# Kernel tuning notes

Hardware: AMD Instinct MI355X
Metric: run time of the kernel (lower is better)

## Reference

```python
import jax, jax.numpy as jnp
import numpy as np

# ---- config (matches init_kwargs) ----
B, N_ENC, COND_REPEAT = 4, 4, 200
BLOCKS, LAYERS_PER = 2, 8
R, S, CC, CLASSES = 128, 128, 64, 256
Q_ZERO = 128
DILATIONS = [2 ** i for i in range(LAYERS_PER)] * BLOCKS  # [1..128, 1..128]
L = len(DILATIONS)


def setup_inputs() -> dict:
    key = jax.random.key(0)
    ks = jax.random.split(key, 12)
    g = lambda k, shape, fan: (jax.random.normal(k, shape, jnp.float32) / np.float32(np.sqrt(fan)))
    return {
        "encodings": jax.random.normal(ks[0], (B, CC, N_ENC), jnp.float32),
        "W_first": g(ks[1], (R, 1, 2), 2.0),            # causal conv 1->R, k=2
        "b_first": jnp.zeros((R,), jnp.float32),
        "Wc": g(ks[2], (L, 2 * R, R, 2), 2.0 * R),       # dilated causal convs R->2R, k=2
        "bc": jnp.zeros((L, 2 * R), jnp.float32),
        "Wcond": g(ks[3], (L, 2 * R, CC), CC),           # per-layer 1x1 cond (no bias)
        "Wres": g(ks[4], (L, R, R), R),                  # per-layer 1x1 residual
        "bres": jnp.zeros((L, R), jnp.float32),
        "Wskip_l": g(ks[5], (L, S, R), R),               # per-layer 1x1 skip
        "bskip_l": jnp.zeros((L, S), jnp.float32),
        "Wskip0": g(ks[6], (S, R), R),                   # top skip_conv
        "bskip0": jnp.zeros((S,), jnp.float32),
        "Wcond_top": g(ks[7], (S, CC), CC),              # top 1x1 cond (no bias)
        "Wfc": g(ks[8], (S, S), S),
        "bfc": jnp.zeros((S,), jnp.float32),
        "Wlogits": g(ks[9], (CLASSES, S), S),
        "blogits": jnp.zeros((CLASSES,), jnp.float32),
    }


def reference(encodings, W_first, b_first, Wc, bc, Wcond, Wres, bres,
              Wskip_l, bskip_l, Wskip0, bskip0, Wcond_top, Wfc, bfc,
              Wlogits, blogits):
    """Autoregressive WaveNet generation with per-layer dilated-conv queues.
    Returns per-step logits [B, CLASSES, T] (sampling uses argmax, method='max')."""
    T = N_ENC * COND_REPEAT
    # each encoding frame conditions cond_repeat consecutive samples
    c_seq = jnp.repeat(encodings, COND_REPEAT, axis=2).transpose(2, 0, 1)  # [T,B,CC]

    def step(carry, c_t):
        sample, fq, queues = carry  # sample:[B] int, fq:[B] (first-conv queue), queues: tuple of [B,R,d_l]
        x = sample.astype(jnp.float32) / 127.5 - 1.0  # mu-law index -> [-1, 1]
        # first causal conv (k=2): past value from queue, current value x
        res = fq[:, None] * W_first[:, 0, 0] + x[:, None] * W_first[:, 0, 1] + b_first  # [B,R]
        skip = res @ Wskip0.T + bskip0  # [B,S]
        new_queues = []
        for l in range(L):  # fixed structural loop over layers
            q = queues[l]  # [B,R,d_l]; q[:,:,0] is the input from d_l steps ago
            z = q[:, :, 0] @ Wc[l, :, :, 0].T + res @ Wc[l, :, :, 1].T + bc[l]  # [B,2R]
            z = z + c_t @ Wcond[l].T
            gate, out = jnp.split(z, 2, axis=1)
            h = jax.nn.sigmoid(gate) * jnp.tanh(out)
            new_queues.append(jnp.concatenate([q[:, :, 1:], res[:, :, None]], axis=2))
            skip = skip + h @ Wskip_l[l].T + bskip_l[l]
            res = res + h @ Wres[l].T + bres[l]  # residual connection
        s = jax.nn.relu(skip) @ Wfc.T + bfc + c_t @ Wcond_top.T
        logits = jax.nn.relu(s) @ Wlogits.T + blogits  # [B,CLASSES]
        new_sample = jnp.argmax(logits, axis=1).astype(jnp.int32)
        return (new_sample, x, tuple(new_queues)), logits

    carry0 = (jnp.full((B,), Q_ZERO, jnp.int32),
              jnp.zeros((B,), jnp.float32),
              tuple(jnp.zeros((B, R, d), jnp.float32) for d in DILATIONS))
    _, logits = jax.lax.scan(step, carry0, c_seq)
    return logits.transpose(1, 2, 0)  # [B, CLASSES, T]
```

## Files before the change

kernel.cpp:

```cpp
#include <hip/hip_runtime.h>


typedef unsigned long long u64;

#define TSTEPS 800
#define CREP 200

#define CTR_OFF 0
#define ABT_OFF 64
#define RESBOX_OFF 4096
#define BOXB 16384
#define SKIPBOX_OFF (RESBOX_OFF + 4 * BOXB)
#define RING_OFF (SKIPBOX_OFF + 4 * BOXB)
#define RINGB 261120
#define WS_END (RING_OFF + 4 * RINGB)

#define SPIN_LIMIT 1048576

static __device__ __forceinline__ void pub64(u64* p, float x, unsigned tag) {
  const u64 v = (u64)__float_as_uint(x) | ((u64)tag << 32);
  asm volatile("global_atomic_swap_x2 %0, %1, off" ::"v"(p), "v"(v) : "memory");
}
static __device__ __forceinline__ u64 poll64(u64* p) {
  u64 old;
  const u64 z = 0;
  asm volatile("global_atomic_add_x2 %0, %1, %2, off sc0\n\ts_waitcnt vmcnt(0)"
               : "=&v"(old) : "v"(p), "v"(z) : "memory");
  return old;
}
static __device__ __forceinline__ void poll4(u64* p, u64& a, u64& b, u64& c, u64& d) {
  const u64 z = 0;
  asm volatile(
      "global_atomic_add_x2 %0, %4, %5, off sc0\n\t"
      "global_atomic_add_x2 %1, %4, %5, off offset:1024 sc0\n\t"
      "global_atomic_add_x2 %2, %4, %5, off offset:2048 sc0\n\t"
      "global_atomic_add_x2 %3, %4, %5, off offset:3072 sc0\n\t"
      "s_waitcnt vmcnt(0)"
      : "=&v"(a), "=&v"(b), "=&v"(c), "=&v"(d)
      : "v"(p), "v"(z)
      : "memory");
}
static __device__ __forceinline__ unsigned ld32(const unsigned* p) {
  return __hip_atomic_load(p, __ATOMIC_RELAXED, __HIP_MEMORY_SCOPE_AGENT);
}
static __device__ __forceinline__ void st32(unsigned* p, unsigned v) {
  __hip_atomic_store(p, v, __ATOMIC_RELAXED, __HIP_MEMORY_SCOPE_AGENT);
}
static __device__ __forceinline__ float spinf(u64* p, unsigned tag, unsigned* abt) {
  int g = 0;
  for (;;) {
    const u64 v = poll64(p);
    if ((unsigned)(v >> 32) == tag) return __uint_as_float((unsigned)v);
    if (((++g) & 255) == 0) {
      if (g > SPIN_LIMIT || ld32(abt)) { st32(abt, 1u); return 0.f; }
    }
  }
}

__global__ void wn_init(unsigned char* ws) {
  uint4 z; z.x = 0; z.y = 0; z.z = 0; z.w = 0;
  uint4* p = (uint4*)ws;
  const int n = WS_END / 16;
  for (int i = blockIdx.x * blockDim.x + threadIdx.x; i < n; i += gridDim.x * blockDim.x)
    p[i] = z;
}

__global__ __launch_bounds__(512, 2) void wn_main(
    const float* __restrict__ enc, const float* __restrict__ Wfirst,
    const float* __restrict__ bfirst, const float* __restrict__ Wc,
    const float* __restrict__ bcv, const float* __restrict__ Wcond,
    const float* __restrict__ Wres, const float* __restrict__ bres,
    const float* __restrict__ Wskip, const float* __restrict__ bskipl,
    const float* __restrict__ Wskip0, const float* __restrict__ bskip0,
    const float* __restrict__ Wct, const float* __restrict__ Wfcw,
    const float* __restrict__ bfc, const float* __restrict__ Wlg,
    const float* __restrict__ blgg, float* __restrict__ dout,
    unsigned char* __restrict__ ws) {
  __shared__ __attribute__((aligned(16))) unsigned char smem[14336];
  float* zbS = (float*)smem;
  float* ct2 = (float*)smem;
  float* resS = (float*)(smem + 4096);
  float* zpartS = (float*)(smem + 4608);
  float* ppS = (float*)(smem + 6656);
  float* hS = (float*)(smem + 8704);
  float* rpartS = (float*)(smem + 9216);
  float* skpartS = (float*)(smem + 11264);
  float* pastS = (float*)(smem + 13312);
  float* amaxv = (float*)(smem + 13824);
  int* amaxi = (int*)(smem + 13840);
  int* argixS = (int*)(smem + 13856);
  int* roleS = (int*)(smem + 13872);

  const int tid = threadIdx.x;
  unsigned* abt = (unsigned*)(ws + ABT_OFF);

  if (tid == 0) {
    unsigned xcc;
    asm volatile("s_getreg_b32 %0, hwreg(HW_REG_XCC_ID)" : "=s"(xcc));
    int role = 999;
    if (xcc < 4)
      role = (int)__hip_atomic_fetch_add((unsigned*)(ws + CTR_OFF) + xcc, 1u,
                                         __ATOMIC_RELAXED, __HIP_MEMORY_SCOPE_AGENT);
    roleS[0] = role;
    roleS[1] = (int)xcc;
  }
  __syncthreads();
  const int role = roleS[0];
  const int b = roleS[1];
  if (role >= 17) return;

  const int jz = tid & 255, kh = tid >> 8;
  const int j3 = tid & 127, q3 = tid >> 7;

  if (role < 16) {
    const int l = role;
    const int dl = 1 << (l & 7);
    const int pfx = (l < 8) ? ((1 << l) - 1) : (254 + (1 << (l - 8)));

    float wc1h[64], wc0h[64], wresq[32];
    {
      const float4* wbase = (const float4*)(Wc + ((size_t)(l * 256 + jz) * 128 + kh * 64) * 2);
#pragma unroll
      for (int m = 0; m < 32; m++) {
        const float4 v = wbase[m];
        wc0h[2 * m] = v.x; wc1h[2 * m] = v.y;
        wc0h[2 * m + 1] = v.z; wc1h[2 * m + 1] = v.w;
      }
      const float4* rbase = (const float4*)(Wres + (size_t)(l * 128 + j3) * 128 + q3 * 32);
#pragma unroll
      for (int m = 0; m < 8; m++) {
        const float4 v = rbase[m];
        wresq[4 * m] = v.x; wresq[4 * m + 1] = v.y;
        wresq[4 * m + 2] = v.z; wresq[4 * m + 3] = v.w;
      }
    }
    const float bresv = bres[l * 128 + j3];

    if (tid < 256) {
      for (int e = 0; e < 4; e++) {
        float a = bcv[l * 256 + tid];
        for (int c = 0; c < 64; c++)
          a = fmaf(enc[(b * 64 + c) * 4 + e], Wcond[((size_t)l * 256 + tid) * 64 + c], a);
        zbS[e * 256 + tid] = a;
      }
    }
    ppS[tid] = 0.f;

    u64* inbox = (u64*)(ws + RESBOX_OFF + (size_t)b * BOXB) + l * 128;
    u64* outbox = (u64*)(ws + RESBOX_OFF + (size_t)b * BOXB) + ((l + 1) & 15) * 128;
    u64* skipbox = (u64*)(ws + SKIPBOX_OFF + (size_t)b * BOXB) + l * 128;
    float* ringf = (float*)(ws + RING_OFF + (size_t)b * RINGB) + pfx * 128;
    const float4* wskb = (const float4*)(Wskip + (size_t)(l * 128 + j3) * 128 + q3 * 32);
    __syncthreads();

    for (int t = 0; t < TSTEPS; t++) {
      const unsigned want = (unsigned)(t + 1);
      const int e = t / CREP;

      if (tid < 128) resS[tid] = spinf(inbox + tid, want, abt);
      __syncthreads();

      {
        const float* rp = resS + kh * 64;
        float zp = 0.f;
#pragma unroll
        for (int kk = 0; kk < 64; kk++) zp = fmaf(rp[kk], wc1h[kk], zp);
        zpartS[(kh << 8) | jz] = zp;
      }
      __syncthreads();
      if (tid < 128) {
        const float g0 = zpartS[tid] + zpartS[256 + tid] + ppS[tid] + ppS[256 + tid] +
                         zbS[e * 256 + tid];
        const float o0 = zpartS[128 + tid] + zpartS[384 + tid] + ppS[128 + tid] +
                         ppS[384 + tid] + zbS[e * 256 + 128 + tid];
        hS[tid] = (1.f / (1.f + expf(-g0))) * tanhf(o0);
      }
      __syncthreads();

      {
        const float* hp = hS + q3 * 32;
        float rp2 = 0.f;
#pragma unroll
        for (int kk = 0; kk < 32; kk++) rp2 = fmaf(hp[kk], wresq[kk], rp2);
        rpartS[(q3 << 7) | j3] = rp2;
      }
      __syncthreads();
      if (l < 15 && tid < 128)
        pub64(outbox + tid,
              resS[tid] + rpartS[tid] + rpartS[128 + tid] + rpartS[256 + tid] +
                  rpartS[384 + tid] + bresv,
              want);

      {
        const float* hp = hS + q3 * 32;
        float sp = 0.f;
#pragma unroll
        for (int m = 0; m < 8; m++) {
          const float4 wv = wskb[m];
          sp = fmaf(hp[4 * m], wv.x, sp);
          sp = fmaf(hp[4 * m + 1], wv.y, sp);
          sp = fmaf(hp[4 * m + 2], wv.z, sp);
          sp = fmaf(hp[4 * m + 3], wv.w, sp);
        }
        skpartS[(q3 << 7) | j3] = sp;
      }
      __syncthreads();
      if (tid < 128)
        pub64(skipbox + tid,
              skpartS[tid] + skpartS[128 + tid] + skpartS[256 + tid] + skpartS[384 + tid],
              want);

      if (tid < 128) {
        ringf[(t % dl) * 128 + tid] = resS[tid];
        pastS[tid] = (dl == 1) ? resS[tid] : ringf[((t + 1) % dl) * 128 + tid];
      }
      __syncthreads();
      {
        const float* pp2 = pastS + kh * 64;
        float ppn = 0.f;
#pragma unroll
        for (int kk = 0; kk < 64; kk++) ppn = fmaf(pp2[kk], wc0h[kk], ppn);
        ppS[(kh << 8) | jz] = ppn;
      }
    }
  } else {
    float wlgr[64], wfcr[32], wsk0[32];
    {
      const float4* lb = (const float4*)(Wlg + (size_t)jz * 128 + kh * 64);
#pragma unroll
      for (int m = 0; m < 16; m++) {
        const float4 v = lb[m];
        wlgr[4 * m] = v.x; wlgr[4 * m + 1] = v.y;
        wlgr[4 * m + 2] = v.z; wlgr[4 * m + 3] = v.w;
      }
      const float4* fb = (const float4*)(Wfcw + (size_t)j3 * 128 + q3 * 32);
      const float4* sb = (const float4*)(Wskip0 + (size_t)j3 * 128 + q3 * 32);
#pragma unroll
      for (int m = 0; m < 8; m++) {
        const float4 v = fb[m];
        const float4 u = sb[m];
        wfcr[4 * m] = v.x; wfcr[4 * m + 1] = v.y;
        wfcr[4 * m + 2] = v.z; wfcr[4 * m + 3] = v.w;
        wsk0[4 * m] = u.x; wsk0[4 * m + 1] = u.y;
        wsk0[4 * m + 2] = u.z; wsk0[4 * m + 3] = u.w;
      }
    }
    float wf0 = 0.f, wf1 = 0.f, bfv = 0.f, bs0 = 0.f, bsum = 0.f, bfcv = 0.f;
    if (tid < 128) {
      wf0 = Wfirst[2 * tid]; wf1 = Wfirst[2 * tid + 1]; bfv = bfirst[tid];
      bs0 = bskip0[tid];
      for (int l2 = 0; l2 < 16; l2++) bsum += bskipl[l2 * 128 + tid];
      bfcv = bfc[tid];
      for (int e = 0; e < 4; e++) {
        float a = 0.f;
        for (int c = 0; c < 64; c++)
          a = fmaf(enc[(b * 64 + c) * 4 + e], Wct[tid * 64 + c], a);
        ct2[e * 128 + tid] = a;
      }
    }
    const float blgv = (tid < 256) ? blgg[tid] : 0.f;
    float fq = 0.f, x = 128.f / 127.5f - 1.f;
    u64* res0box = (u64*)(ws + RESBOX_OFF + (size_t)b * BOXB);
    u64* skb = (u64*)(ws + SKIPBOX_OFF + (size_t)b * BOXB);
    float* res0S = resS;
    float* partS = zpartS;
    float* lgS = ppS;
    float* skS = hS;
    float* s1S = rpartS;
    __syncthreads();

    for (int t = 0; t < TSTEPS; t++) {
      const unsigned want = (unsigned)(t + 1);
      const int e = t / CREP;

      if (tid < 128) {
        const float rv = fmaf(fq, wf0, fmaf(x, wf1, bfv));
        pub64(res0box + tid, rv, want);
        res0S[tid] = rv;
      }
      __syncthreads();

      {
        const float* rp = res0S + q3 * 32;
        float sp = 0.f;
#pragma unroll
        for (int kk = 0; kk < 32; kk++) sp = fmaf(rp[kk], wsk0[kk], sp);
        partS[tid] = sp;
      }
      __syncthreads();
      if (tid < 128) {
        float sacc = partS[tid] + partS[128 + tid] + partS[256 + tid] + partS[384 + tid] +
                     bs0 + bsum;
        u64 v[16];
        int g = 0;
        for (;;) {
          bool ok = true;
#pragma unroll
          for (int grp = 0; grp < 4; grp++)
            poll4(skb + grp * 512 + tid, v[grp * 4], v[grp * 4 + 1], v[grp * 4 + 2],
                  v[grp * 4 + 3]);
#pragma unroll
          for (int l2 = 0; l2 < 16; l2++) ok &= ((unsigned)(v[l2] >> 32) == want);
          if (ok) break;
          if (((++g) & 63) == 0) {
            if (g > (SPIN_LIMIT >> 6) || ld32(abt)) { st32(abt, 1u); break; }
          }
        }
#pragma unroll
        for (int l2 = 0; l2 < 16; l2++) sacc += __uint_as_float((unsigned)v[l2]);
        skS[tid] = fmaxf(sacc, 0.f);
      }
      __syncthreads();

      {
        const float* sp2 = skS + q3 * 32;
        float p = 0.f;
#pragma unroll
        for (int kk = 0; kk < 32; kk++) p = fmaf(sp2[kk], wfcr[kk], p);
        partS[tid] = p;
      }
      __syncthreads();
      if (tid < 128)
        s1S[tid] = fmaxf(partS[tid] + partS[128 + tid] + partS[256 + tid] +
                             partS[384 + tid] + bfcv + ct2[e * 128 + tid],
                         0.f);
      __syncthreads();

      {
        const float* sp3 = s1S + kh * 64;
        float p = 0.f;
#pragma unroll
        for (int kk = 0; kk < 64; kk++) p = fmaf(sp3[kk], wlgr[kk], p);
        lgS[(kh << 8) | jz] = p;
      }
      __syncthreads();

      float lg = 0.f;
      if (tid < 256) lg = lgS[tid] + lgS[256 + tid] + blgv;

      {
        float bv = lg;
        int bi = tid;
#pragma unroll
        for (int off = 32; off >= 1; off >>= 1) {
          const float ov = __shfl_down(bv, (unsigned)off);
          const int oi = __shfl_down(bi, (unsigned)off);
          if (ov > bv || (ov == bv && oi < bi)) { bv = ov; bi = oi; }
        }
        if (tid < 256 && (tid & 63) == 0) { amaxv[tid >> 6] = bv; amaxi[tid >> 6] = bi; }
      }
      __syncthreads();
      if (tid == 0) {
        float bb = amaxv[0];
        int ii = amaxi[0];
        for (int w2 = 1; w2 < 4; w2++)
          if (amaxv[w2] > bb || (amaxv[w2] == bb && amaxi[w2] < ii)) {
            bb = amaxv[w2]; ii = amaxi[w2];
          }
        argixS[0] = ii;
      }
      __syncthreads();
      fq = x;
      x = (float)argixS[0] / 127.5f - 1.f;

      if (tid < 256) dout[((size_t)b * 256 + tid) * TSTEPS + t] = lg;
    }
  }
}

extern "C" void kernel_launch(void* const* d_in, const int* in_sizes, int n_in,
                              void* d_out, int out_size, void* d_ws, size_t ws_size,
                              hipStream_t stream) {
  (void)in_sizes; (void)n_in; (void)out_size; (void)ws_size;
  wn_init<<<256, 256, 0, stream>>>((unsigned char*)d_ws);
  wn_main<<<1024, 512, 0, stream>>>(
      (const float*)d_in[0], (const float*)d_in[1], (const float*)d_in[2],
      (const float*)d_in[3], (const float*)d_in[4], (const float*)d_in[5],
      (const float*)d_in[6], (const float*)d_in[7], (const float*)d_in[8],
      (const float*)d_in[9], (const float*)d_in[10], (const float*)d_in[11],
      (const float*)d_in[12], (const float*)d_in[13], (const float*)d_in[14],
      (const float*)d_in[15], (const float*)d_in[16],
      (float*)d_out, (unsigned char*)d_ws);
}
```

Before: 23.72 ms.

## Use 1024-thread blocks, move dilation ring to LDS, merge per-step barrier phases

Each per-layer workgroup now has 1024 threads, which halves the per-thread dot-product lengths, and the past-input ring buffer moves from global workspace into shared memory. The residual and skip projections, together with the next step's past-input conv partials, are fused into a single phase. This cuts the number of __syncthreads per time step on the serial critical path. The costs are a larger LDS footprint (64KB ring) and eight-way partial reductions in place of four.

```diff
diff --git a/kernel.cpp b/kernel.cpp
--- a/kernel.cpp
+++ b/kernel.cpp
@@ -11,9 +11,7 @@
 #define RESBOX_OFF 4096
 #define BOXB 16384
 #define SKIPBOX_OFF (RESBOX_OFF + 4 * BOXB)
-#define RING_OFF (SKIPBOX_OFF + 4 * BOXB)
-#define RINGB 261120
-#define WS_END (RING_OFF + 4 * RINGB)
+#define WS_END (SKIPBOX_OFF + 4 * BOXB)
 
 #define SPIN_LIMIT 1048576
 
@@ -65,7 +63,7 @@
     p[i] = z;
 }
 
-__global__ __launch_bounds__(512, 2) void wn_main(
+__global__ __launch_bounds__(1024, 4) void wn_main(
     const float* __restrict__ enc, const float* __restrict__ Wfirst,
     const float* __restrict__ bfirst, const float* __restrict__ Wc,
     const float* __restrict__ bcv, const float* __restrict__ Wcond,
@@ -76,20 +74,19 @@
     const float* __restrict__ bfc, const float* __restrict__ Wlg,
     const float* __restrict__ blgg, float* __restrict__ dout,
     unsigned char* __restrict__ ws) {
-  __shared__ __attribute__((aligned(16))) unsigned char smem[14336];
-  float* zbS = (float*)smem;
-  float* ct2 = (float*)smem;
-  float* resS = (float*)(smem + 4096);
-  float* zpartS = (float*)(smem + 4608);
-  float* ppS = (float*)(smem + 6656);
-  float* hS = (float*)(smem + 8704);
-  float* rpartS = (float*)(smem + 9216);
-  float* skpartS = (float*)(smem + 11264);
-  float* pastS = (float*)(smem + 13312);
-  float* amaxv = (float*)(smem + 13824);
-  int* amaxi = (int*)(smem + 13840);
-  int* argixS = (int*)(smem + 13856);
-  int* roleS = (int*)(smem + 13872);
+  __shared__ float ringS[128 * 128];
+  __shared__ float zbS[1024];
+  __shared__ float resS[128];
+  __shared__ float zpartS[1024];
+  __shared__ float ppS[1024];
+  __shared__ float hS[128];
+  __shared__ float rpartS[1024];
+  __shared__ float skpartS[1024];
+  __shared__ float pastS[128];
+  __shared__ float amaxv[4];
+  __shared__ int amaxi[4];
+  __shared__ int argixS[1];
+  __shared__ int roleS[2];
 
   const int tid = threadIdx.x;
   unsigned* abt = (unsigned*)(ws + ABT_OFF);
@@ -109,29 +106,32 @@
   const int b = roleS[1];
   if (role >= 17) return;
 
-  const int jz = tid & 255, kh = tid >> 8;
-  const int j3 = tid & 127, q3 = tid >> 7;
+  const int jz = tid & 255, qz = tid >> 8;
+  const int j3 = tid & 127, q8 = tid >> 7;
 
   if (role < 16) {
     const int l = role;
     const int dl = 1 << (l & 7);
-    const int pfx = (l < 8) ? ((1 << l) - 1) : (254 + (1 << (l - 8)));
-
-    float wc1h[64], wc0h[64], wresq[32];
+
+    float wc0q[32], wc1q[32], wresr[16], wskipr[16];
     {
-      const float4* wbase = (const float4*)(Wc + ((size_t)(l * 256 + jz) * 128 + kh * 64) * 2);
-#pragma unroll
-      for (int m = 0; m < 32; m++) {
-        const float4 v = wbase[m];
-        wc0h[2 * m] = v.x; wc1h[2 * m] = v.y;
-        wc0h[2 * m + 1] = v.z; wc1h[2 * m + 1] = v.w;
-      }
-      const float4* rbase = (const float4*)(Wres + (size_t)(l * 128 + j3) * 128 + q3 * 32);
-#pragma unroll
-      for (int m = 0; m < 8; m++) {
-        const float4 v = rbase[m];
-        wresq[4 * m] = v.x; wresq[4 * m + 1] = v.y;
-        wresq[4 * m + 2] = v.z; wresq[4 * m + 3] = v.w;
+      const float2* wcb = (const float2*)Wc + ((size_t)(l * 256 + jz) * 128 + qz * 32);
+#pragma unroll
+      for (int kk = 0; kk < 32; kk++) {
+        const float2 v = wcb[kk];
+        wc0q[kk] = v.x;
+        wc1q[kk] = v.y;
+      }
+      const float4* rb = (const float4*)(Wres + (size_t)(l * 128 + j3) * 128 + q8 * 16);
+      const float4* sb = (const float4*)(Wskip + (size_t)(l * 128 + j3) * 128 + q8 * 16);
+#pragma unroll
+      for (int m = 0; m < 4; m++) {
+        const float4 v = rb[m];
+        const float4 u = sb[m];
+        wresr[4 * m] = v.x; wresr[4 * m + 1] = v.y;
+        wresr[4 * m + 2] = v.z; wresr[4 * m + 3] = v.w;
+        wskipr[4 * m] = u.x; wskipr[4 * m + 1] = u.y;
+        wskipr[4 * m + 2] = u.z; wskipr[4 * m + 3] = u.w;
       }
     }
     const float bresv = bres[l * 128 + j3];
@@ -144,13 +144,12 @@
         zbS[e * 256 + tid] = a;
       }
     }
+    for (int i = tid; i < 128 * 128; i += 1024) ringS[i] = 0.f;
     ppS[tid] = 0.f;
 
     u64* inbox = (u64*)(ws + RESBOX_OFF + (size_t)b * BOXB) + l * 128;
     u64* outbox = (u64*)(ws + RESBOX_OFF + (size_t)b * BOXB) + ((l + 1) & 15) * 128;
     u64* skipbox = (u64*)(ws + SKIPBOX_OFF + (size_t)b * BOXB) + l * 128;
-    float* ringf = (float*)(ws + RING_OFF + (size_t)b * RINGB) + pfx * 128;
-    const float4* wskb = (const float4*)(Wskip + (size_t)(l * 128 + j3) * 128 + q3 * 32);
     __syncthreads();
 
     for (int t = 0; t < TSTEPS; t++) {
@@ -161,88 +160,79 @@
       __syncthreads();
 
       {
-        const float* rp = resS + kh * 64;
+        const float* rp = resS + qz * 32;
         float zp = 0.f;
 #pragma unroll
-        for (int kk = 0; kk < 64; kk++) zp = fmaf(rp[kk], wc1h[kk], zp);
-        zpartS[(kh << 8) | jz] = zp;
-      }
-      __syncthreads();
-      if (tid < 128) {
-        const float g0 = zpartS[tid] + zpartS[256 + tid] + ppS[tid] + ppS[256 + tid] +
-                         zbS[e * 256 + tid];
-        const float o0 = zpartS[128 + tid] + zpartS[384 + tid] + ppS[128 + tid] +
-                         ppS[384 + tid] + zbS[e * 256 + 128 + tid];
+        for (int kk = 0; kk < 32; kk++) zp = fmaf(rp[kk], wc1q[kk], zp);
+        zpartS[tid] = zp;
+      }
+      __syncthreads();
+
+      if (tid < 128) {
+        const float g0 = zpartS[tid] + zpartS[256 + tid] + zpartS[512 + tid] +
+                         zpartS[768 + tid] + ppS[tid] + ppS[256 + tid] + ppS[512 + tid] +
+                         ppS[768 + tid] + zbS[e * 256 + tid];
+        const int to = 128 + tid;
+        const float o0 = zpartS[to] + zpartS[256 + to] + zpartS[512 + to] +
+                         zpartS[768 + to] + ppS[to] + ppS[256 + to] + ppS[512 + to] +
+                         ppS[768 + to] + zbS[e * 256 + to];
         hS[tid] = (1.f / (1.f + expf(-g0))) * tanhf(o0);
-      }
-      __syncthreads();
-
-      {
-        const float* hp = hS + q3 * 32;
-        float rp2 = 0.f;
-#pragma unroll
-        for (int kk = 0; kk < 32; kk++) rp2 = fmaf(hp[kk], wresq[kk], rp2);
-        rpartS[(q3 << 7) | j3] = rp2;
-      }
-      __syncthreads();
-      if (l < 15 && tid < 128)
-        pub64(outbox + tid,
-              resS[tid] + rpartS[tid] + rpartS[128 + tid] + rpartS[256 + tid] +
-                  rpartS[384 + tid] + bresv,
-              want);
-
-      {
-        const float* hp = hS + q3 * 32;
-        float sp = 0.f;
-#pragma unroll
-        for (int m = 0; m < 8; m++) {
-          const float4 wv = wskb[m];
-          sp = fmaf(hp[4 * m], wv.x, sp);
-          sp = fmaf(hp[4 * m + 1], wv.y, sp);
-          sp = fmaf(hp[4 * m + 2], wv.z, sp);
-          sp = fmaf(hp[4 * m + 3], wv.w, sp);
+        ringS[(t % dl) * 128 + tid] = resS[tid];
+        pastS[tid] = (dl == 1) ? resS[tid] : ringS[((t + 1) % dl) * 128 + tid];
+      }
+      __syncthreads();
+
+      {
+        const float* hp = hS + q8 * 16;
+        float rp2 = 0.f, sp = 0.f;
+#pragma unroll
+        for (int kk = 0; kk < 16; kk++) {
+          rp2 = fmaf(hp[kk], wresr[kk], rp2);
+          sp = fmaf(hp[kk], wskipr[kk], sp);
         }
-        skpartS[(q3 << 7) | j3] = sp;
-      }
-      __syncthreads();
-      if (tid < 128)
-        pub64(skipbox + tid,
-              skpartS[tid] + skpartS[128 + tid] + skpartS[256 + tid] + skpartS[384 + tid],
-              want);
-
-      if (tid < 128) {
-        ringf[(t % dl) * 128 + tid] = resS[tid];
-        pastS[tid] = (dl == 1) ? resS[tid] : ringf[((t + 1) % dl) * 128 + tid];
-      }
-      __syncthreads();
-      {
-        const float* pp2 = pastS + kh * 64;
+        rpartS[tid] = rp2;
+        skpartS[tid] = sp;
+        const float* pq = pastS + qz * 32;
         float ppn = 0.f;
 #pragma unroll
-        for (int kk = 0; kk < 64; kk++) ppn = fmaf(pp2[kk], wc0h[kk], ppn);
-        ppS[(kh << 8) | jz] = ppn;
+        for (int kk = 0; kk < 32; kk++) ppn = fmaf(pq[kk], wc0q[kk], ppn);
+        ppS[tid] = ppn;
+      }
+      __syncthreads();
+
+      if (tid < 128) {
+        if (l < 15) {
+          float rsum = resS[tid] + bresv;
+#pragma unroll
+          for (int q = 0; q < 8; q++) rsum += rpartS[q * 128 + tid];
+          pub64(outbox + tid, rsum, want);
+        }
+        float ssum = 0.f;
+#pragma unroll
+        for (int q = 0; q < 8; q++) ssum += skpartS[q * 128 + tid];
+        pub64(skipbox + tid, ssum, want);
       }
     }
   } else {
-    float wlgr[64], wfcr[32], wsk0[32];
+    float wlgr[32], wfcr[16], wsk0r[16];
     {
-      const float4* lb = (const float4*)(Wlg + (size_t)jz * 128 + kh * 64);
-#pragma unroll
-      for (int m = 0; m < 16; m++) {
+      const float4* lb = (const float4*)(Wlg + (size_t)jz * 128 + qz * 32);
+#pragma unroll
+      for (int m = 0; m < 8; m++) {
         const float4 v = lb[m];
         wlgr[4 * m] = v.x; wlgr[4 * m + 1] = v.y;
         wlgr[4 * m + 2] = v.z; wlgr[4 * m + 3] = v.w;
       }
-      const float4* fb = (const float4*)(Wfcw + (size_t)j3 * 128 + q3 * 32);
-      const float4* sb = (const float4*)(Wskip0 + (size_t)j3 * 128 + q3 * 32);
-#pragma unroll
-      for (int m = 0; m < 8; m++) {
+      const float4* fb = (const float4*)(Wfcw + (size_t)j3 * 128 + q8 * 16);
+      const float4* s0b = (const float4*)(Wskip0 + (size_t)j3 * 128 + q8 * 16);
+#pragma unroll
+      for (int m = 0; m < 4; m++) {
         const float4 v = fb[m];
-        const float4 u = sb[m];
+        const float4 u = s0b[m];
         wfcr[4 * m] = v.x; wfcr[4 * m + 1] = v.y;
         wfcr[4 * m + 2] = v.z; wfcr[4 * m + 3] = v.w;
-        wsk0[4 * m] = u.x; wsk0[4 * m + 1] = u.y;
-        wsk0[4 * m + 2] = u.z; wsk0[4 * m + 3] = u.w;
+        wsk0r[4 * m] = u.x; wsk0r[4 * m + 1] = u.y;
+        wsk0r[4 * m + 2] = u.z; wsk0r[4 * m + 3] = u.w;
       }
     }
     float wf0 = 0.f, wf1 = 0.f, bfv = 0.f, bs0 = 0.f, bsum = 0.f, bfcv = 0.f;
@@ -255,18 +245,13 @@
         float a = 0.f;
         for (int c = 0; c < 64; c++)
           a = fmaf(enc[(b * 64 + c) * 4 + e], Wct[tid * 64 + c], a);
-        ct2[e * 128 + tid] = a;
+        zbS[e * 128 + tid] = a;
       }
     }
     const float blgv = (tid < 256) ? blgg[tid] : 0.f;
     float fq = 0.f, x = 128.f / 127.5f - 1.f;
     u64* res0box = (u64*)(ws + RESBOX_OFF + (size_t)b * BOXB);
     u64* skb = (u64*)(ws + SKIPBOX_OFF + (size_t)b * BOXB);
-    float* res0S = resS;
-    float* partS = zpartS;
-    float* lgS = ppS;
-    float* skS = hS;
-    float* s1S = rpartS;
     __syncthreads();
 
     for (int t = 0; t < TSTEPS; t++) {
@@ -276,21 +261,23 @@
       if (tid < 128) {
         const float rv = fmaf(fq, wf0, fmaf(x, wf1, bfv));
         pub64(res0box + tid, rv, want);
-        res0S[tid] = rv;
-      }
-      __syncthreads();
-
-      {
-        const float* rp = res0S + q3 * 32;
+        resS[tid] = rv;
+      }
+      __syncthreads();
+
+      {
+        const float* rp = resS + q8 * 16;
         float sp = 0.f;
 #pragma unroll
-        for (int kk = 0; kk < 32; kk++) sp = fmaf(rp[kk], wsk0[kk], sp);
-        partS[tid] = sp;
-      }
-      __syncthreads();
-      if (tid < 128) {
-        float sacc = partS[tid] + partS[128 + tid] + partS[256 + tid] + partS[384 + tid] +
-                     bs0 + bsum;
+        for (int kk = 0; kk < 16; kk++) sp = fmaf(rp[kk], wsk0r[kk], sp);
+        zpartS[tid] = sp;
+      }
+      __syncthreads();
+
+      if (tid < 128) {
+        float sacc = bs0 + bsum;
+#pragma unroll
+        for (int q = 0; q < 8; q++) sacc += zpartS[q * 128 + tid];
         u64 v[16];
         int g = 0;
         for (;;) {
@@ -308,37 +295,39 @@
         }
 #pragma unroll
         for (int l2 = 0; l2 < 16; l2++) sacc += __uint_as_float((unsigned)v[l2]);
-        skS[tid] = fmaxf(sacc, 0.f);
-      }
-      __syncthreads();
-
-      {
-        const float* sp2 = skS + q3 * 32;
+        hS[tid] = fmaxf(sacc, 0.f);
+      }
+      __syncthreads();
+
+      {
+        const float* sp2 = hS + q8 * 16;
         float p = 0.f;
 #pragma unroll
-        for (int kk = 0; kk < 32; kk++) p = fmaf(sp2[kk], wfcr[kk], p);
-        partS[tid] = p;
-      }
-      __syncthreads();
-      if (tid < 128)
-        s1S[tid] = fmaxf(partS[tid] + partS[128 + tid] + partS[256 + tid] +
-                             partS[384 + tid] + bfcv + ct2[e * 128 + tid],
-                         0.f);
-      __syncthreads();
-
-      {
-        const float* sp3 = s1S + kh * 64;
+        for (int kk = 0; kk < 16; kk++) p = fmaf(sp2[kk], wfcr[kk], p);
+        zpartS[tid] = p;
+      }
+      __syncthreads();
+
+      if (tid < 128) {
+        float p = bfcv + zbS[e * 128 + tid];
+#pragma unroll
+        for (int q = 0; q < 8; q++) p += zpartS[q * 128 + tid];
+        pastS[tid] = fmaxf(p, 0.f);
+      }
+      __syncthreads();
+
+      {
+        const float* sp3 = pastS + qz * 32;
         float p = 0.f;
 #pragma unroll
-        for (int kk = 0; kk < 64; kk++) p = fmaf(sp3[kk], wlgr[kk], p);
-        lgS[(kh << 8) | jz] = p;
+        for (int kk = 0; kk < 32; kk++) p = fmaf(sp3[kk], wlgr[kk], p);
+        ppS[tid] = p;
       }
       __syncthreads();
 
       float lg = 0.f;
-      if (tid < 256) lg = lgS[tid] + lgS[256 + tid] + blgv;
-
-      {
+      if (tid < 256) {
+        lg = ppS[tid] + ppS[256 + tid] + ppS[512 + tid] + ppS[768 + tid] + blgv;
         float bv = lg;
         int bi = tid;
 #pragma unroll
@@ -347,7 +336,7 @@
           const int oi = __shfl_down(bi, (unsigned)off);
           if (ov > bv || (ov == bv && oi < bi)) { bv = ov; bi = oi; }
         }
-        if (tid < 256 && (tid & 63) == 0) { amaxv[tid >> 6] = bv; amaxi[tid >> 6] = bi; }
+        if ((tid & 63) == 0) { amaxv[tid >> 6] = bv; amaxi[tid >> 6] = bi; }
       }
       __syncthreads();
       if (tid == 0) {
@@ -372,8 +361,8 @@
                               void* d_out, int out_size, void* d_ws, size_t ws_size,
                               hipStream_t stream) {
   (void)in_sizes; (void)n_in; (void)out_size; (void)ws_size;
-  wn_init<<<256, 256, 0, stream>>>((unsigned char*)d_ws);
-  wn_main<<<1024, 512, 0, stream>>>(
+  wn_init<<<64, 256, 0, stream>>>((unsigned char*)d_ws);
+  wn_main<<<512, 1024, 0, stream>>>(
       (const float*)d_in[0], (const float*)d_in[1], (const float*)d_in[2],
       (const float*)d_in[3], (const float*)d_in[4], (const float*)d_in[5],
       (const float*)d_in[6], (const float*)d_in[7], (const float*)d_in[8],
```

After: 29.19 ms. 1.23x slower.
